# Kernel optimization log

Measured on AMD Instinct MI355X. Metric: run time of the kernel, lower is better.

## Reference

```python
import jax, jax.numpy as jnp
import numpy as np

N_HEAD = 16


def setup_inputs() -> dict:
    key = jax.random.key(0)
    k1, k2, k3 = jax.random.split(key, 3)
    B, T, C = 2, 2048, 1024
    x = jax.random.normal(k1, (B, T, C), dtype=jnp.float32)
    w_attn = jax.random.normal(k2, (C, 3 * C), dtype=jnp.float32) * 0.02
    w_proj = jax.random.normal(k3, (C, C), dtype=jnp.float32) * 0.02
    return {"x": x, "w_attn": w_attn, "w_proj": w_proj}


def reference(x, w_attn, w_proj):
    B, T, C = x.shape
    H = N_HEAD
    D = C // H
    qkv = x @ w_attn  # [B, T, 3C]
    q, k, v = jnp.split(qkv, 3, axis=2)
    q = q.reshape(B, T, H, D)
    k = k.reshape(B, T, H, D)
    v = v.reshape(B, T, H, D)
    scale = 1.0 / jnp.sqrt(jnp.asarray(D, dtype=x.dtype))
    # Full T x T score matrix, matching the 'standard_attention' path.
    att = jnp.einsum('bthd,bshd->bhts', q, k) * scale  # [B, H, T, T]
    causal = jnp.tril(jnp.ones((T, T), dtype=bool))
    att = jnp.where(causal[None, None, :, :], att, jnp.asarray(-jnp.inf, dtype=att.dtype))
    att = jax.nn.softmax(att, axis=-1)
    # dropout_p is False (== 0.0) in the original module, so no dropout applied.
    y = jnp.einsum('bhts,bshd->bthd', att, v)  # [B, T, H, D]
    y = y.reshape(B, T, C)
    return y @ w_proj
```

## Files before the change

kernel.cpp:

```cpp
#include <hip/hip_runtime.h>
#include <hip/hip_bf16.h>
#include <math.h>

#define BB 2
#define TT 2048
#define HH 16
#define DD 64
#define CC 1024
#define C3 3072

typedef __attribute__((ext_vector_type(8))) short bf16x8;
typedef __attribute__((ext_vector_type(4))) short bf16x4;
typedef __attribute__((ext_vector_type(4))) float f32x4;
typedef __attribute__((ext_vector_type(2))) unsigned int u32x2;

__device__ __forceinline__ unsigned short f2bf(float f) {
  union { float f; unsigned u; } v; v.f = f;
  unsigned r = v.u + 0x7fffu + ((v.u >> 16) & 1u);
  return (unsigned short)(r >> 16);
}
__device__ __forceinline__ unsigned pack2bf(float a, float b) {
  __hip_bfloat162 h = __float22bfloat162_rn(make_float2(a, b));
  union { __hip_bfloat162 h; unsigned u; } cv; cv.h = h;
  return cv.u;
}

__device__ __forceinline__ void async_cp16(const void* g, void* l) {
  __builtin_amdgcn_global_load_lds(
      (const __attribute__((address_space(1))) void*)g,
      (__attribute__((address_space(3))) void*)l, 16, 0, 0);
}

__global__ __launch_bounds__(256)
void prep(const float* __restrict__ x, const float* __restrict__ w_attn,
          const float* __restrict__ w_proj, unsigned short* __restrict__ xb,
          unsigned short* __restrict__ wat, unsigned short* __restrict__ wpt) {
  __shared__ __align__(16) float Ts[64][68];
  const int bx = blockIdx.x, tid = threadIdx.x;
  if (bx < 1024) {
    int i = bx * 256 + tid;
#pragma unroll
    for (int it = 0; it < 4; ++it, i += 262144) {
      const float4 v = ((const float4*)x)[i];
      bf16x4 o = {(short)f2bf(v.x), (short)f2bf(v.y),
                  (short)f2bf(v.z), (short)f2bf(v.w)};
      ((bf16x4*)xb)[i] = o;
    }
    return;
  }
  const float* W;
  unsigned short* WT;
  int Nd, bound, n0, k0;
  float s;
  if (bx < 1792) {
    const int bid = bx - 1024;
    W = w_attn; WT = wat; Nd = 3072; bound = 1024; s = 0.18033688f;
    n0 = (bid % 48) * 64; k0 = (bid / 48) * 64;
  } else {
    const int bid = bx - 1792;
    W = w_proj; WT = wpt; Nd = 1024; bound = 0; s = 1.0f;
    n0 = (bid % 16) * 64; k0 = (bid / 16) * 64;
  }
  const int rl = tid >> 4, c4 = tid & 15;
#pragma unroll
  for (int it = 0; it < 4; ++it) {
    const int r = it * 16 + rl;
    *(float4*)&Ts[r][c4 * 4] =
        *(const float4*)(W + (size_t)(k0 + r) * Nd + n0 + c4 * 4);
  }
  __syncthreads();
#pragma unroll
  for (int it = 0; it < 4; ++it) {
    const int n = it * 16 + rl;
    const float sc = (n0 + n < bound) ? s : 1.0f;
    bf16x4 o = {(short)f2bf(Ts[c4 * 4 + 0][n] * sc),
                (short)f2bf(Ts[c4 * 4 + 1][n] * sc),
                (short)f2bf(Ts[c4 * 4 + 2][n] * sc),
                (short)f2bf(Ts[c4 * 4 + 3][n] * sc)};
    *(bf16x4*)(WT + (size_t)(n0 + n) * CC + k0 + c4 * 4) = o;
  }
}

__global__ __launch_bounds__(256, 3)
void gemm_qkv(const unsigned short* __restrict__ A,
              const unsigned short* __restrict__ BT,
              unsigned short* __restrict__ Cb,
              unsigned short* __restrict__ Vout) {
  __shared__ __align__(16) unsigned short As[2 * 128 * 32];
  __shared__ __align__(16) unsigned short Bs[2 * 128 * 32];

  const int tid = threadIdx.x;
  const int w = tid >> 6, lane = tid & 63;
  const int l15 = lane & 15, quad = lane >> 4;
  const int wm = w >> 1, wn = w & 1;
  const int row0 = blockIdx.y * 128, col0 = blockIdx.x * 128;

  const int ca0 = tid, ca1 = tid + 256;
  const int ra0 = ca0 >> 2, ka0 = ((ca0 & 3) ^ ((ca0 >> 3) & 3)) * 8;
  const int ra1 = ca1 >> 2, ka1 = ((ca1 & 3) ^ ((ca1 >> 3) & 3)) * 8;
  const unsigned short* gA0 = A + (size_t)(row0 + ra0) * CC + ka0;
  const unsigned short* gA1 = A + (size_t)(row0 + ra1) * CC + ka1;
  const unsigned short* gB0 = BT + (size_t)(col0 + ra0) * CC + ka0;
  const unsigned short* gB1 = BT + (size_t)(col0 + ra1) * CC + ka1;
  const int la0 = tid * 16, la1 = tid * 16 + 4096;

  const int fro = l15 * 64 + 16 * (quad ^ ((l15 >> 1) & 3));

  f32x4 acc[4][4];
#pragma unroll
  for (int i = 0; i < 4; ++i)
#pragma unroll
    for (int j = 0; j < 4; ++j) acc[i][j] = (f32x4){0.f, 0.f, 0.f, 0.f};

  async_cp16(gA0, (char*)As + la0);
  async_cp16(gA1, (char*)As + la1);
  async_cp16(gB0, (char*)Bs + la0);
  async_cp16(gB1, (char*)Bs + la1);

  for (int i = 0; i < 32; ++i) {
    const int cur = i & 1;
    __syncthreads();

    if (i + 1 < 32) {
      const int k1 = (i + 1) * 32;
      const int ab = (cur ^ 1) * 8192;
      async_cp16(gA0 + k1, (char*)As + ab + la0);
      async_cp16(gA1 + k1, (char*)As + ab + la1);
      async_cp16(gB0 + k1, (char*)Bs + ab + la0);
      async_cp16(gB1 + k1, (char*)Bs + ab + la1);
    }

    const char* fA = (const char*)As + cur * 8192 + wm * 4096 + fro;
    const char* fB = (const char*)Bs + cur * 8192 + wn * 4096 + fro;

    bf16x8 af[4], bf[4];
#pragma unroll
    for (int mt = 0; mt < 4; ++mt) af[mt] = *(const bf16x8*)(fA + mt * 1024);
#pragma unroll
    for (int nt = 0; nt < 4; ++nt) bf[nt] = *(const bf16x8*)(fB + nt * 1024);
#pragma unroll
    for (int mt = 0; mt < 4; ++mt)
#pragma unroll
      for (int nt = 0; nt < 4; ++nt)
        acc[mt][nt] = __builtin_amdgcn_mfma_f32_16x16x32_bf16(
            af[mt], bf[nt], acc[mt][nt], 0, 0, 0);
  }

  if (col0 >= 2048) {
#pragma unroll
    for (int mt = 0; mt < 4; ++mt) {
      const int rbase = row0 + wm * 64 + mt * 16 + quad * 4;
      const int bq = rbase >> 11, t0 = rbase & 2047;
#pragma unroll
      for (int nt = 0; nt < 4; ++nt) {
        const int d = col0 + wn * 64 + nt * 16 + l15 - 2048;
        bf16x4 o = {(short)f2bf(acc[mt][nt][0]), (short)f2bf(acc[mt][nt][1]),
                    (short)f2bf(acc[mt][nt][2]), (short)f2bf(acc[mt][nt][3])};
        *(bf16x4*)(Vout + (((size_t)(bq << 10) + d) << 11) + t0) = o;
      }
    }
  } else {
#pragma unroll
    for (int mt = 0; mt < 4; ++mt) {
      const int rbase = row0 + wm * 64 + mt * 16 + quad * 4;
#pragma unroll
      for (int r = 0; r < 4; ++r) {
        unsigned short* cr =
            Cb + (size_t)(rbase + r) * C3 + col0 + wn * 64 + l15;
#pragma unroll
        for (int nt = 0; nt < 4; ++nt) cr[nt * 16] = f2bf(acc[mt][nt][r]);
      }
    }
  }
}

__global__ __launch_bounds__(256, 2)
void gemm_out(const unsigned short* __restrict__ A,
              const unsigned short* __restrict__ BT,
              float* __restrict__ Cf) {
  __shared__ __align__(16) unsigned short As[2 * 64 * 64];
  __shared__ __align__(16) unsigned short Bs[2 * 128 * 64];

  const int tid = threadIdx.x;
  const int w = tid >> 6, lane = tid & 63;
  const int l15 = lane & 15, quad = lane >> 4;
  const int wm = w >> 1, wn = w & 1;
  const int row0 = blockIdx.y * 64, col0 = blockIdx.x * 128;

  const int ca0 = tid, ca1 = tid + 256;
  const int ra0 = ca0 >> 3, ka0 = ((ca0 & 7) ^ ((ca0 >> 3) & 7)) * 8;
  const int ra1 = ca1 >> 3, ka1 = ((ca1 & 7) ^ ((ca1 >> 3) & 7)) * 8;
  const unsigned short* gA0 = A + (size_t)(row0 + ra0) * CC + ka0;
  const unsigned short* gA1 = A + (size_t)(row0 + ra1) * CC + ka1;
  const unsigned short* gB[4];
  int lb[4];
#pragma unroll
  for (int t = 0; t < 4; ++t) {
    const int c = tid + t * 256;
    const int rb = c >> 3, kb = ((c & 7) ^ ((c >> 3) & 7)) * 8;
    gB[t] = BT + (size_t)(col0 + rb) * CC + kb;
    lb[t] = c * 16;
  }
  const int la0 = tid * 16, la1 = tid * 16 + 4096;

  const int fro = l15 * 128 + ((quad ^ (l15 & 7)) << 4);

  f32x4 acc[2][4];
#pragma unroll
  for (int i = 0; i < 2; ++i)
#pragma unroll
    for (int j = 0; j < 4; ++j) acc[i][j] = (f32x4){0.f, 0.f, 0.f, 0.f};

  async_cp16(gA0, (char*)As + la0);
  async_cp16(gA1, (char*)As + la1);
#pragma unroll
  for (int t = 0; t < 4; ++t) async_cp16(gB[t], (char*)Bs + lb[t]);

  for (int i = 0; i < 16; ++i) {
    const int cur = i & 1;
    __syncthreads();

    if (i + 1 < 16) {
      const int k1 = (i + 1) * 64;
      const int ab = (cur ^ 1) * 8192, bb = (cur ^ 1) * 16384;
      async_cp16(gA0 + k1, (char*)As + ab + la0);
      async_cp16(gA1 + k1, (char*)As + ab + la1);
#pragma unroll
      for (int t = 0; t < 4; ++t) async_cp16(gB[t] + k1, (char*)Bs + bb + lb[t]);
    }

    const char* fA = (const char*)As + cur * 8192 + wm * 4096 + fro;
    const char* fB = (const char*)Bs + cur * 16384 + wn * 8192 + fro;

#pragma unroll
    for (int kh = 0; kh < 2; ++kh) {
      const int xo = kh * 64;
      bf16x8 af[2], bf[4];
#pragma unroll
      for (int mt = 0; mt < 2; ++mt)
        af[mt] = *(const bf16x8*)(fA + mt * 2048 + ((fro + xo) & 127) - (fro & 127));
#pragma unroll
      for (int nt = 0; nt < 4; ++nt)
        bf[nt] = *(const bf16x8*)(fB + nt * 2048 + ((fro + xo) & 127) - (fro & 127));
#pragma unroll
      for (int mt = 0; mt < 2; ++mt)
#pragma unroll
        for (int nt = 0; nt < 4; ++nt)
          acc[mt][nt] = __builtin_amdgcn_mfma_f32_16x16x32_bf16(
              af[mt], bf[nt], acc[mt][nt], 0, 0, 0);
    }
  }

#pragma unroll
  for (int mt = 0; mt < 2; ++mt) {
    const int rbase = row0 + wm * 32 + mt * 16 + quad * 4;
#pragma unroll
    for (int r = 0; r < 4; ++r) {
      float* cr = Cf + (size_t)(rbase + r) * CC + col0 + wn * 64 + l15;
#pragma unroll
      for (int nt = 0; nt < 4; ++nt) cr[nt * 16] = acc[mt][nt][r];
    }
  }
}

__global__ __launch_bounds__(256)
void attn_mfma(const unsigned short* __restrict__ qkvb,
               const unsigned short* __restrict__ vt,
               unsigned short* __restrict__ y) {
  const int n = blockIdx.x;
  const int bh = (n & 7) + 8 * ((n >> 3) & 3);
  const int qpair = n >> 5;
  const int b = bh >> 4, h = bh & 15;
  const int tid = threadIdx.x;
  const int w = tid >> 6;
  const int lane = tid & 63;
  const int l15 = lane & 15, quad = lane >> 4;

  __shared__ __align__(16) char Kb[2 * 8192];
  __shared__ __align__(16) char Vb[2 * 8192];
  __shared__ __align__(16) unsigned short Ps[4 * 16 * 72];
  char* psw = (char*)(Ps + w * 16 * 72);

  const int lr = lane >> 3;
  const int lc = lane & 7;
  const int srcoff = ((lc ^ lr) << 4);
  const char* ksrc = (const char*)qkvb + ((size_t)(b * TT) * C3 + 1024 + h * 64) * 2;
  const char* vsrc = (const char*)vt + ((size_t)(b * HH + h) * DD * TT) * 2;

  const int fro = l15 * 128 + ((quad ^ (l15 & 7)) << 4);

  const int psrow = l15 * 144;

  bf16x8 onesf;
#pragma unroll
  for (int jj = 0; jj < 8; ++jj) onesf[jj] = (short)0x3F80;

  for (int phase = 0; phase < 2; ++phase) {
    const int qt = phase == 0 ? 31 - qpair : qpair;

    if (phase) __syncthreads();

    const unsigned short* qrow =
        qkvb + (size_t)(b * TT + qt * 64 + w * 16 + l15) * C3 + h * DD;
    bf16x8 qf0 = *(const bf16x8*)(qrow + quad * 8);
    bf16x8 qf1 = *(const bf16x8*)(qrow + 32 + quad * 8);

    f32x4 O[4];
#pragma unroll
    for (int dt = 0; dt < 4; ++dt) O[dt] = (f32x4){0.f, 0.f, 0.f, 0.f};
    f32x4 lacc = (f32x4){0.f, 0.f, 0.f, 0.f};

#pragma unroll
    for (int i = 0; i < 2; ++i) {
      async_cp16(ksrc + (size_t)(w * 16 + i * 8 + lr) * (C3 * 2) + srcoff,
                 Kb + w * 2048 + i * 1024);
      async_cp16(vsrc + (size_t)(w * 16 + i * 8 + lr) * (TT * 2) + srcoff,
                 Vb + w * 2048 + i * 1024);
    }

    for (int j = 0; j <= qt; ++j) {
      const int cur = j & 1;
      __syncthreads();

      if (j < qt) {
        const int key1 = (j + 1) * 64;
        char* kd = Kb + (cur ^ 1) * 8192 + w * 2048;
        char* vd = Vb + (cur ^ 1) * 8192 + w * 2048;
#pragma unroll
        for (int i = 0; i < 2; ++i) {
          async_cp16(
              ksrc + (size_t)(key1 + w * 16 + i * 8 + lr) * (C3 * 2) + srcoff,
              kd + i * 1024);
          async_cp16(
              vsrc + (size_t)(w * 16 + i * 8 + lr) * (TT * 2) + key1 * 2 + srcoff,
              vd + i * 1024);
        }
      }

      const char* Kc = Kb + cur * 8192;
      const char* Vc = Vb + cur * 8192;

      f32x4 S[4];
#pragma unroll
      for (int ct = 0; ct < 4; ++ct) {
        bf16x8 k0 = *(const bf16x8*)(Kc + ct * 2048 + fro);
        bf16x8 k1 = *(const bf16x8*)(Kc + ct * 2048 + (fro ^ 64));
        f32x4 z = (f32x4){-12.f, -12.f, -12.f, -12.f};
        z = __builtin_amdgcn_mfma_f32_16x16x32_bf16(k0, qf0, z, 0, 0, 0);
        z = __builtin_amdgcn_mfma_f32_16x16x32_bf16(k1, qf1, z, 0, 0, 0);
        S[ct] = z;
      }

      if (j == qt) {
#pragma unroll
        for (int ct = 0; ct < 4; ++ct)
#pragma unroll
          for (int r = 0; r < 4; ++r)
            if (16 * ct + quad * 4 + r > w * 16 + l15) S[ct][r] = -INFINITY;
      }

#pragma unroll
      for (int ct = 0; ct < 4; ++ct) {
        u32x2 d;
        d[0] = pack2bf(__builtin_amdgcn_exp2f(S[ct][0]),
                       __builtin_amdgcn_exp2f(S[ct][1]));
        d[1] = pack2bf(__builtin_amdgcn_exp2f(S[ct][2]),
                       __builtin_amdgcn_exp2f(S[ct][3]));
        *(u32x2*)(psw + psrow + (((ct + l15) & 3) << 5) + quad * 8) = d;
      }

      bf16x8 pf0, pf1;
      {
        const int c0 = (quad >> 1), c1 = 2 + (quad >> 1);
        pf0 = *(const bf16x8*)(psw + psrow + (((c0 + l15) & 3) << 5) + ((quad & 1) << 4));
        pf1 = *(const bf16x8*)(psw + psrow + (((c1 + l15) & 3) << 5) + ((quad & 1) << 4));
      }

      lacc = __builtin_amdgcn_mfma_f32_16x16x32_bf16(onesf, pf0, lacc, 0, 0, 0);
      lacc = __builtin_amdgcn_mfma_f32_16x16x32_bf16(onesf, pf1, lacc, 0, 0, 0);
#pragma unroll
      for (int dt = 0; dt < 4; ++dt) {
        bf16x8 v0 = *(const bf16x8*)(Vc + dt * 2048 + fro);
        bf16x8 v1 = *(const bf16x8*)(Vc + dt * 2048 + (fro ^ 64));
        O[dt] = __builtin_amdgcn_mfma_f32_16x16x32_bf16(v0, pf0, O[dt], 0, 0, 0);
        O[dt] = __builtin_amdgcn_mfma_f32_16x16x32_bf16(v1, pf1, O[dt], 0, 0, 0);
      }
    }

    const float inv = 1.0f / lacc[0];
    unsigned short* yr =
        y + (size_t)(b * TT + qt * 64 + w * 16 + l15) * CC + h * DD + quad * 4;
#pragma unroll
    for (int dt = 0; dt < 4; ++dt) {
      bf16x4 o = {(short)f2bf(O[dt][0] * inv), (short)f2bf(O[dt][1] * inv),
                  (short)f2bf(O[dt][2] * inv), (short)f2bf(O[dt][3] * inv)};
      *(bf16x4*)(yr + dt * 16) = o;
    }
  }
}

extern "C" void kernel_launch(void* const* d_in, const int* in_sizes, int n_in,
                              void* d_out, int out_size, void* d_ws,
                              size_t ws_size, hipStream_t stream) {
  const float* x      = (const float*)d_in[0];
  const float* w_attn = (const float*)d_in[1];
  const float* w_proj = (const float*)d_in[2];
  float* out = (float*)d_out;

  unsigned short* xb   = (unsigned short*)d_ws;
  unsigned short* wat  = xb + (size_t)4096 * 1024;
  unsigned short* wpt  = wat + (size_t)3072 * 1024;
  unsigned short* qkvb = wpt + (size_t)1024 * 1024;
  unsigned short* vt   = qkvb + (size_t)4096 * 3072;
  unsigned short* yb   = vt + (size_t)BB * HH * DD * TT;

  dim3 blk(256);

  prep<<<2048, blk, 0, stream>>>(x, w_attn, w_proj, xb, wat, wpt);

  gemm_qkv<<<dim3(C3 / 128, (BB * TT) / 128), blk, 0, stream>>>(
      xb, wat, qkvb, vt);

  attn_mfma<<<dim3(512, 1, 1), blk, 0, stream>>>(qkvb, vt, yb);

  gemm_out<<<dim3(CC / 128, (BB * TT) / 64), blk, 0, stream>>>(yb, wpt, out);
}
```

Baseline: 170.2 us.

## Split attention keys across warps with register K/V loads and LDS reduction

Restructures the attention kernel so each warp handles all 64 query rows of the tile but only every fourth 32-key chunk. K and V fragments come straight from global memory into registers, with K double-buffered in registers, replacing the shared-memory async copy pipeline and its per-iteration block barriers. The four warps' partial O and row sums are then combined through a two-level shared-memory reduction before warp 0 normalises and writes the output. This removes a __syncthreads per key tile but raises register pressure (O is now 4x4 accumulators per warp), adds an end-of-phase reduction, and makes every warp read K/V from global memory rather than sharing a single staged copy.

```diff
diff --git a/kernel.cpp b/kernel.cpp
--- a/kernel.cpp
+++ b/kernel.cpp
@@ -263,7 +263,72 @@
   }
 }
 
-__global__ __launch_bounds__(256)
+__device__ __forceinline__ void attn_chunk(
+    const int c, const int qt, const int l15, const int quad,
+    const bf16x8 (&kf)[2][2], const bf16x8 (&qf)[4][2], const bf16x8 onesf,
+    const unsigned short* __restrict__ vbase, char* psw, const int psrow,
+    f32x4 (&O)[4][4], f32x4 (&lacc)[4]) {
+  bf16x8 vf[4];
+#pragma unroll
+  for (int dt = 0; dt < 4; ++dt)
+    vf[dt] = *(const bf16x8*)(vbase + (size_t)dt * 16 * TT + 32 * c);
+
+  f32x4 S[2][4];
+#pragma unroll
+  for (int ks = 0; ks < 2; ++ks)
+#pragma unroll
+    for (int qs = 0; qs < 4; ++qs) {
+      f32x4 z = (f32x4){-12.f, -12.f, -12.f, -12.f};
+      z = __builtin_amdgcn_mfma_f32_16x16x32_bf16(kf[ks][0], qf[qs][0], z, 0, 0, 0);
+      z = __builtin_amdgcn_mfma_f32_16x16x32_bf16(kf[ks][1], qf[qs][1], z, 0, 0, 0);
+      S[ks][qs] = z;
+    }
+
+  if (c >= 2 * qt) {
+#pragma unroll
+    for (int ks = 0; ks < 2; ++ks)
+#pragma unroll
+      for (int qs = 0; qs < 4; ++qs)
+#pragma unroll
+        for (int r = 0; r < 4; ++r)
+          if (32 * c + ks * 16 + quad * 4 + r > qt * 64 + qs * 16 + l15)
+            S[ks][qs][r] = -INFINITY;
+  }
+
+#pragma unroll
+  for (int ks = 0; ks < 2; ++ks)
+#pragma unroll
+    for (int qs = 0; qs < 4; ++qs) {
+      u32x2 d;
+      d[0] = pack2bf(__builtin_amdgcn_exp2f(S[ks][qs][0]),
+                     __builtin_amdgcn_exp2f(S[ks][qs][1]));
+      d[1] = pack2bf(__builtin_amdgcn_exp2f(S[ks][qs][2]),
+                     __builtin_amdgcn_exp2f(S[ks][qs][3]));
+      *(u32x2*)(psw + qs * 2304 + psrow + (((ks + l15) & 3) << 5) + quad * 8) = d;
+    }
+
+#pragma unroll
+  for (int qs = 0; qs < 4; ++qs) {
+    const bf16x8 pf = *(const bf16x8*)(psw + qs * 2304 + psrow +
+                                       ((((quad >> 1) + l15) & 3) << 5) +
+                                       ((quad & 1) << 4));
+    lacc[qs] = __builtin_amdgcn_mfma_f32_16x16x32_bf16(onesf, pf, lacc[qs], 0, 0, 0);
+#pragma unroll
+    for (int dt = 0; dt < 4; ++dt)
+      O[dt][qs] = __builtin_amdgcn_mfma_f32_16x16x32_bf16(vf[dt], pf, O[dt][qs], 0, 0, 0);
+  }
+}
+
+#define LOADK(dst, cc)                                                   \
+  do {                                                                   \
+    const unsigned short* kp = kbase + (size_t)(32 * (cc)) * C3;         \
+    dst[0][0] = *(const bf16x8*)(kp);                                    \
+    dst[0][1] = *(const bf16x8*)(kp + 32);                               \
+    dst[1][0] = *(const bf16x8*)(kp + 16 * C3);                          \
+    dst[1][1] = *(const bf16x8*)(kp + 16 * C3 + 32);                     \
+  } while (0)
+
+__global__ __launch_bounds__(256, 2)
 void attn_mfma(const unsigned short* __restrict__ qkvb,
                const unsigned short* __restrict__ vt,
                unsigned short* __restrict__ y) {
@@ -276,125 +341,125 @@
   const int lane = tid & 63;
   const int l15 = lane & 15, quad = lane >> 4;
 
-  __shared__ __align__(16) char Kb[2 * 8192];
-  __shared__ __align__(16) char Vb[2 * 8192];
-  __shared__ __align__(16) unsigned short Ps[4 * 16 * 72];
-  char* psw = (char*)(Ps + w * 16 * 72);
-
-  const int lr = lane >> 3;
-  const int lc = lane & 7;
-  const int srcoff = ((lc ^ lr) << 4);
-  const char* ksrc = (const char*)qkvb + ((size_t)(b * TT) * C3 + 1024 + h * 64) * 2;
-  const char* vsrc = (const char*)vt + ((size_t)(b * HH + h) * DD * TT) * 2;
-
-  const int fro = l15 * 128 + ((quad ^ (l15 & 7)) << 4);
-
+  __shared__ __align__(16) unsigned short Ps[4 * 4 * 16 * 72];
+  __shared__ __align__(16) float Red[2][16][256];
+  __shared__ float Red2[2][4][16];
+
+  char* psw = (char*)Ps + w * (4 * 2304);
   const int psrow = l15 * 144;
+  const int epoff = l15 * 64 + ((quad ^ (l15 & 3)) << 4);
+
+  const unsigned short* kbase =
+      qkvb + (size_t)(b * TT + l15) * C3 + 1024 + h * DD + quad * 8;
+  const unsigned short* vbase =
+      vt + (size_t)(bh * DD + l15) * TT + quad * 8;
 
   bf16x8 onesf;
 #pragma unroll
   for (int jj = 0; jj < 8; ++jj) onesf[jj] = (short)0x3F80;
 
   for (int phase = 0; phase < 2; ++phase) {
-    const int qt = phase == 0 ? 31 - qpair : qpair;
-
-    if (phase) __syncthreads();
-
-    const unsigned short* qrow =
-        qkvb + (size_t)(b * TT + qt * 64 + w * 16 + l15) * C3 + h * DD;
-    bf16x8 qf0 = *(const bf16x8*)(qrow + quad * 8);
-    bf16x8 qf1 = *(const bf16x8*)(qrow + 32 + quad * 8);
-
-    f32x4 O[4];
-#pragma unroll
-    for (int dt = 0; dt < 4; ++dt) O[dt] = (f32x4){0.f, 0.f, 0.f, 0.f};
-    f32x4 lacc = (f32x4){0.f, 0.f, 0.f, 0.f};
-
-#pragma unroll
-    for (int i = 0; i < 2; ++i) {
-      async_cp16(ksrc + (size_t)(w * 16 + i * 8 + lr) * (C3 * 2) + srcoff,
-                 Kb + w * 2048 + i * 1024);
-      async_cp16(vsrc + (size_t)(w * 16 + i * 8 + lr) * (TT * 2) + srcoff,
-                 Vb + w * 2048 + i * 1024);
-    }
-
-    for (int j = 0; j <= qt; ++j) {
-      const int cur = j & 1;
-      __syncthreads();
-
-      if (j < qt) {
-        const int key1 = (j + 1) * 64;
-        char* kd = Kb + (cur ^ 1) * 8192 + w * 2048;
-        char* vd = Vb + (cur ^ 1) * 8192 + w * 2048;
-#pragma unroll
-        for (int i = 0; i < 2; ++i) {
-          async_cp16(
-              ksrc + (size_t)(key1 + w * 16 + i * 8 + lr) * (C3 * 2) + srcoff,
-              kd + i * 1024);
-          async_cp16(
-              vsrc + (size_t)(w * 16 + i * 8 + lr) * (TT * 2) + key1 * 2 + srcoff,
-              vd + i * 1024);
+    const int qt = phase ? qpair : 31 - qpair;
+    const int nc = 2 * (qt + 1);
+
+    const unsigned short* qbase =
+        qkvb + (size_t)(b * TT + qt * 64 + l15) * C3 + h * DD + quad * 8;
+    bf16x8 qf[4][2];
+#pragma unroll
+    for (int qs = 0; qs < 4; ++qs)
+#pragma unroll
+      for (int kh = 0; kh < 2; ++kh)
+        qf[qs][kh] = *(const bf16x8*)(qbase + qs * 16 * C3 + kh * 32);
+
+    f32x4 O[4][4];
+    f32x4 lacc[4];
+#pragma unroll
+    for (int dt = 0; dt < 4; ++dt)
+#pragma unroll
+      for (int qs = 0; qs < 4; ++qs) O[dt][qs] = (f32x4){0.f, 0.f, 0.f, 0.f};
+#pragma unroll
+    for (int qs = 0; qs < 4; ++qs) lacc[qs] = (f32x4){0.f, 0.f, 0.f, 0.f};
+
+    bf16x8 kfA[2][2], kfB[2][2];
+    int c = w;
+    if (c < nc) {
+      LOADK(kfA, c);
+      while (true) {
+        int cn = c + 4;
+        if (cn < nc) LOADK(kfB, cn);
+        attn_chunk(c, qt, l15, quad, kfA, qf, onesf, vbase, psw, psrow, O, lacc);
+        c = cn;
+        if (c >= nc) break;
+        cn = c + 4;
+        if (cn < nc) LOADK(kfA, cn);
+        attn_chunk(c, qt, l15, quad, kfB, qf, onesf, vbase, psw, psrow, O, lacc);
+        c = cn;
+        if (c >= nc) break;
+      }
+    }
+
+    __syncthreads();
+    if (w & 1) {
+      char* rs = (char*)Red + (w >> 1) * 16384;
+#pragma unroll
+      for (int dt = 0; dt < 4; ++dt)
+#pragma unroll
+        for (int qs = 0; qs < 4; ++qs)
+          *(f32x4*)(rs + (dt * 4 + qs) * 1024 + epoff) = O[dt][qs];
+      if (quad == 0) {
+#pragma unroll
+        for (int qs = 0; qs < 4; ++qs) Red2[w >> 1][qs][l15] = lacc[qs][0];
+      }
+    }
+    __syncthreads();
+    float lsum[4];
+#pragma unroll
+    for (int qs = 0; qs < 4; ++qs) lsum[qs] = lacc[qs][0];
+    if (!(w & 1)) {
+      char* rs = (char*)Red + (w >> 1) * 16384;
+#pragma unroll
+      for (int dt = 0; dt < 4; ++dt)
+#pragma unroll
+        for (int qs = 0; qs < 4; ++qs)
+          O[dt][qs] += *(const f32x4*)(rs + (dt * 4 + qs) * 1024 + epoff);
+#pragma unroll
+      for (int qs = 0; qs < 4; ++qs) lsum[qs] += Red2[w >> 1][qs][l15];
+    }
+    __syncthreads();
+    if (w == 2) {
+      char* rs = (char*)Red;
+#pragma unroll
+      for (int dt = 0; dt < 4; ++dt)
+#pragma unroll
+        for (int qs = 0; qs < 4; ++qs)
+          *(f32x4*)(rs + (dt * 4 + qs) * 1024 + epoff) = O[dt][qs];
+      if (quad == 0) {
+#pragma unroll
+        for (int qs = 0; qs < 4; ++qs) Red2[0][qs][l15] = lsum[qs];
+      }
+    }
+    __syncthreads();
+    if (w == 0) {
+      char* rs = (char*)Red;
+#pragma unroll
+      for (int dt = 0; dt < 4; ++dt)
+#pragma unroll
+        for (int qs = 0; qs < 4; ++qs)
+          O[dt][qs] += *(const f32x4*)(rs + (dt * 4 + qs) * 1024 + epoff);
+      unsigned short* yr =
+          y + (size_t)(b * TT + qt * 64 + l15) * CC + h * DD + quad * 4;
+#pragma unroll
+      for (int qs = 0; qs < 4; ++qs) {
+        const float inv = 1.0f / (lsum[qs] + Red2[0][qs][l15]);
+#pragma unroll
+        for (int dt = 0; dt < 4; ++dt) {
+          bf16x4 o = {(short)f2bf(O[dt][qs][0] * inv),
+                      (short)f2bf(O[dt][qs][1] * inv),
+                      (short)f2bf(O[dt][qs][2] * inv),
+                      (short)f2bf(O[dt][qs][3] * inv)};
+          *(bf16x4*)(yr + (size_t)qs * 16 * CC + dt * 16) = o;
         }
       }
-
-      const char* Kc = Kb + cur * 8192;
-      const char* Vc = Vb + cur * 8192;
-
-      f32x4 S[4];
-#pragma unroll
-      for (int ct = 0; ct < 4; ++ct) {
-        bf16x8 k0 = *(const bf16x8*)(Kc + ct * 2048 + fro);
-        bf16x8 k1 = *(const bf16x8*)(Kc + ct * 2048 + (fro ^ 64));
-        f32x4 z = (f32x4){-12.f, -12.f, -12.f, -12.f};
-        z = __builtin_amdgcn_mfma_f32_16x16x32_bf16(k0, qf0, z, 0, 0, 0);
-        z = __builtin_amdgcn_mfma_f32_16x16x32_bf16(k1, qf1, z, 0, 0, 0);
-        S[ct] = z;
-      }
-
-      if (j == qt) {
-#pragma unroll
-        for (int ct = 0; ct < 4; ++ct)
-#pragma unroll
-          for (int r = 0; r < 4; ++r)
-            if (16 * ct + quad * 4 + r > w * 16 + l15) S[ct][r] = -INFINITY;
-      }
-
-#pragma unroll
-      for (int ct = 0; ct < 4; ++ct) {
-        u32x2 d;
-        d[0] = pack2bf(__builtin_amdgcn_exp2f(S[ct][0]),
-                       __builtin_amdgcn_exp2f(S[ct][1]));
-        d[1] = pack2bf(__builtin_amdgcn_exp2f(S[ct][2]),
-                       __builtin_amdgcn_exp2f(S[ct][3]));
-        *(u32x2*)(psw + psrow + (((ct + l15) & 3) << 5) + quad * 8) = d;
-      }
-
-      bf16x8 pf0, pf1;
-      {
-        const int c0 = (quad >> 1), c1 = 2 + (quad >> 1);
-        pf0 = *(const bf16x8*)(psw + psrow + (((c0 + l15) & 3) << 5) + ((quad & 1) << 4));
-        pf1 = *(const bf16x8*)(psw + psrow + (((c1 + l15) & 3) << 5) + ((quad & 1) << 4));
-      }
-
-      lacc = __builtin_amdgcn_mfma_f32_16x16x32_bf16(onesf, pf0, lacc, 0, 0, 0);
-      lacc = __builtin_amdgcn_mfma_f32_16x16x32_bf16(onesf, pf1, lacc, 0, 0, 0);
-#pragma unroll
-      for (int dt = 0; dt < 4; ++dt) {
-        bf16x8 v0 = *(const bf16x8*)(Vc + dt * 2048 + fro);
-        bf16x8 v1 = *(const bf16x8*)(Vc + dt * 2048 + (fro ^ 64));
-        O[dt] = __builtin_amdgcn_mfma_f32_16x16x32_bf16(v0, pf0, O[dt], 0, 0, 0);
-        O[dt] = __builtin_amdgcn_mfma_f32_16x16x32_bf16(v1, pf1, O[dt], 0, 0, 0);
-      }
-    }
-
-    const float inv = 1.0f / lacc[0];
-    unsigned short* yr =
-        y + (size_t)(b * TT + qt * 64 + w * 16 + l15) * CC + h * DD + quad * 4;
-#pragma unroll
-    for (int dt = 0; dt < 4; ++dt) {
-      bf16x4 o = {(short)f2bf(O[dt][0] * inv), (short)f2bf(O[dt][1] * inv),
-                  (short)f2bf(O[dt][2] * inv), (short)f2bf(O[dt][3] * inv)};
-      *(bf16x4*)(yr + dt * 16) = o;
     }
   }
 }
```

After: 173.8 us. +2.2%, slower.

## Use 128-query attention blocks with 8 waves instead of paired 64-query phases

Applied to the files above, without the earlier changes.

The attention kernel now launches 512-thread blocks where 8 waves each own 16 query rows, covering a 128-row query tile that shares one K/V stream. This replaces the two-phase pairing of a long and a short 64-row tile per block. Each wave loads only one 8-row slice of K/V per stage, and waves past their causal limit skip compute. Blocks are ordered so that heavy and light query tiles are interleaved. The aim is to halve K/V traffic per query and raise occupancy, at the cost of idle waves on the diagonal tiles and coarser per-block load balance.

```diff
diff --git a/kernel.cpp b/kernel.cpp
--- a/kernel.cpp
+++ b/kernel.cpp
@@ -263,13 +263,14 @@
   }
 }
 
-__global__ __launch_bounds__(256)
+__global__ __launch_bounds__(512, 4)
 void attn_mfma(const unsigned short* __restrict__ qkvb,
                const unsigned short* __restrict__ vt,
                unsigned short* __restrict__ y) {
   const int n = blockIdx.x;
   const int bh = (n & 7) + 8 * ((n >> 3) & 3);
-  const int qpair = n >> 5;
+  const int m = n >> 5;
+  const int qb = (m < 8) ? m : 23 - m;
   const int b = bh >> 4, h = bh & 15;
   const int tid = threadIdx.x;
   const int w = tid >> 6;
@@ -278,8 +279,10 @@
 
   __shared__ __align__(16) char Kb[2 * 8192];
   __shared__ __align__(16) char Vb[2 * 8192];
-  __shared__ __align__(16) unsigned short Ps[4 * 16 * 72];
-  char* psw = (char*)(Ps + w * 16 * 72);
+  __shared__ __align__(16) unsigned short Ps[8 * 16 * 72];
+
+  char* psw = (char*)Ps + w * 2304;
+  const int psrow = l15 * 144;
 
   const int lr = lane >> 3;
   const int lc = lane & 7;
@@ -289,113 +292,99 @@
 
   const int fro = l15 * 128 + ((quad ^ (l15 & 7)) << 4);
 
-  const int psrow = l15 * 144;
-
   bf16x8 onesf;
 #pragma unroll
   for (int jj = 0; jj < 8; ++jj) onesf[jj] = (short)0x3F80;
 
-  for (int phase = 0; phase < 2; ++phase) {
-    const int qt = phase == 0 ? 31 - qpair : qpair;
-
-    if (phase) __syncthreads();
-
-    const unsigned short* qrow =
-        qkvb + (size_t)(b * TT + qt * 64 + w * 16 + l15) * C3 + h * DD;
-    bf16x8 qf0 = *(const bf16x8*)(qrow + quad * 8);
-    bf16x8 qf1 = *(const bf16x8*)(qrow + 32 + quad * 8);
-
-    f32x4 O[4];
-#pragma unroll
-    for (int dt = 0; dt < 4; ++dt) O[dt] = (f32x4){0.f, 0.f, 0.f, 0.f};
-    f32x4 lacc = (f32x4){0.f, 0.f, 0.f, 0.f};
-
-#pragma unroll
-    for (int i = 0; i < 2; ++i) {
-      async_cp16(ksrc + (size_t)(w * 16 + i * 8 + lr) * (C3 * 2) + srcoff,
-                 Kb + w * 2048 + i * 1024);
-      async_cp16(vsrc + (size_t)(w * 16 + i * 8 + lr) * (TT * 2) + srcoff,
-                 Vb + w * 2048 + i * 1024);
-    }
-
-    for (int j = 0; j <= qt; ++j) {
-      const int cur = j & 1;
-      __syncthreads();
-
-      if (j < qt) {
-        const int key1 = (j + 1) * 64;
-        char* kd = Kb + (cur ^ 1) * 8192 + w * 2048;
-        char* vd = Vb + (cur ^ 1) * 8192 + w * 2048;
-#pragma unroll
-        for (int i = 0; i < 2; ++i) {
-          async_cp16(
-              ksrc + (size_t)(key1 + w * 16 + i * 8 + lr) * (C3 * 2) + srcoff,
-              kd + i * 1024);
-          async_cp16(
-              vsrc + (size_t)(w * 16 + i * 8 + lr) * (TT * 2) + key1 * 2 + srcoff,
-              vd + i * 1024);
-        }
-      }
-
-      const char* Kc = Kb + cur * 8192;
-      const char* Vc = Vb + cur * 8192;
-
-      f32x4 S[4];
-#pragma unroll
-      for (int ct = 0; ct < 4; ++ct) {
-        bf16x8 k0 = *(const bf16x8*)(Kc + ct * 2048 + fro);
-        bf16x8 k1 = *(const bf16x8*)(Kc + ct * 2048 + (fro ^ 64));
-        f32x4 z = (f32x4){-12.f, -12.f, -12.f, -12.f};
-        z = __builtin_amdgcn_mfma_f32_16x16x32_bf16(k0, qf0, z, 0, 0, 0);
-        z = __builtin_amdgcn_mfma_f32_16x16x32_bf16(k1, qf1, z, 0, 0, 0);
-        S[ct] = z;
-      }
-
-      if (j == qt) {
-#pragma unroll
-        for (int ct = 0; ct < 4; ++ct)
-#pragma unroll
-          for (int r = 0; r < 4; ++r)
-            if (16 * ct + quad * 4 + r > w * 16 + l15) S[ct][r] = -INFINITY;
-      }
-
-#pragma unroll
-      for (int ct = 0; ct < 4; ++ct) {
-        u32x2 d;
-        d[0] = pack2bf(__builtin_amdgcn_exp2f(S[ct][0]),
-                       __builtin_amdgcn_exp2f(S[ct][1]));
-        d[1] = pack2bf(__builtin_amdgcn_exp2f(S[ct][2]),
-                       __builtin_amdgcn_exp2f(S[ct][3]));
-        *(u32x2*)(psw + psrow + (((ct + l15) & 3) << 5) + quad * 8) = d;
-      }
-
-      bf16x8 pf0, pf1;
-      {
-        const int c0 = (quad >> 1), c1 = 2 + (quad >> 1);
-        pf0 = *(const bf16x8*)(psw + psrow + (((c0 + l15) & 3) << 5) + ((quad & 1) << 4));
-        pf1 = *(const bf16x8*)(psw + psrow + (((c1 + l15) & 3) << 5) + ((quad & 1) << 4));
-      }
-
-      lacc = __builtin_amdgcn_mfma_f32_16x16x32_bf16(onesf, pf0, lacc, 0, 0, 0);
-      lacc = __builtin_amdgcn_mfma_f32_16x16x32_bf16(onesf, pf1, lacc, 0, 0, 0);
-#pragma unroll
-      for (int dt = 0; dt < 4; ++dt) {
-        bf16x8 v0 = *(const bf16x8*)(Vc + dt * 2048 + fro);
-        bf16x8 v1 = *(const bf16x8*)(Vc + dt * 2048 + (fro ^ 64));
-        O[dt] = __builtin_amdgcn_mfma_f32_16x16x32_bf16(v0, pf0, O[dt], 0, 0, 0);
-        O[dt] = __builtin_amdgcn_mfma_f32_16x16x32_bf16(v1, pf1, O[dt], 0, 0, 0);
-      }
-    }
-
-    const float inv = 1.0f / lacc[0];
-    unsigned short* yr =
-        y + (size_t)(b * TT + qt * 64 + w * 16 + l15) * CC + h * DD + quad * 4;
+  const int nt = 2 * qb + 2;
+  const int qrow_my = qb * 128 + w * 16 + l15;
+  const int jlast = (qb * 128 + w * 16 + 15) >> 6;
+
+  const unsigned short* qrow =
+      qkvb + (size_t)(b * TT + qb * 128 + w * 16 + l15) * C3 + h * DD;
+  bf16x8 qf0 = *(const bf16x8*)(qrow + quad * 8);
+  bf16x8 qf1 = *(const bf16x8*)(qrow + 32 + quad * 8);
+
+  f32x4 O[4];
+#pragma unroll
+  for (int dt = 0; dt < 4; ++dt) O[dt] = (f32x4){0.f, 0.f, 0.f, 0.f};
+  f32x4 lacc = (f32x4){0.f, 0.f, 0.f, 0.f};
+
+  async_cp16(ksrc + (size_t)(w * 8 + lr) * (C3 * 2) + srcoff, Kb + w * 1024);
+  async_cp16(vsrc + (size_t)(w * 8 + lr) * (TT * 2) + srcoff, Vb + w * 1024);
+
+  for (int j = 0; j < nt; ++j) {
+    const int cur = j & 1;
+    __syncthreads();
+
+    if (j + 1 < nt) {
+      const int key1 = (j + 1) * 64;
+      async_cp16(ksrc + (size_t)(key1 + w * 8 + lr) * (C3 * 2) + srcoff,
+                 Kb + (cur ^ 1) * 8192 + w * 1024);
+      async_cp16(vsrc + (size_t)(w * 8 + lr) * (TT * 2) + key1 * 2 + srcoff,
+                 Vb + (cur ^ 1) * 8192 + w * 1024);
+    }
+
+    if (j > jlast) continue;
+
+    const char* Kc = Kb + cur * 8192;
+    const char* Vc = Vb + cur * 8192;
+
+    f32x4 S[4];
+#pragma unroll
+    for (int ct = 0; ct < 4; ++ct) {
+      bf16x8 k0 = *(const bf16x8*)(Kc + ct * 2048 + fro);
+      bf16x8 k1 = *(const bf16x8*)(Kc + ct * 2048 + (fro ^ 64));
+      f32x4 z = (f32x4){-12.f, -12.f, -12.f, -12.f};
+      z = __builtin_amdgcn_mfma_f32_16x16x32_bf16(k0, qf0, z, 0, 0, 0);
+      z = __builtin_amdgcn_mfma_f32_16x16x32_bf16(k1, qf1, z, 0, 0, 0);
+      S[ct] = z;
+    }
+
+    if (j == jlast) {
+#pragma unroll
+      for (int ct = 0; ct < 4; ++ct)
+#pragma unroll
+        for (int r = 0; r < 4; ++r)
+          if (64 * j + 16 * ct + quad * 4 + r > qrow_my) S[ct][r] = -INFINITY;
+    }
+
+#pragma unroll
+    for (int ct = 0; ct < 4; ++ct) {
+      u32x2 d;
+      d[0] = pack2bf(__builtin_amdgcn_exp2f(S[ct][0]),
+                     __builtin_amdgcn_exp2f(S[ct][1]));
+      d[1] = pack2bf(__builtin_amdgcn_exp2f(S[ct][2]),
+                     __builtin_amdgcn_exp2f(S[ct][3]));
+      *(u32x2*)(psw + psrow + (((ct + l15) & 3) << 5) + quad * 8) = d;
+    }
+
+    bf16x8 pf0, pf1;
+    {
+      const int c0 = (quad >> 1), c1 = 2 + (quad >> 1);
+      pf0 = *(const bf16x8*)(psw + psrow + (((c0 + l15) & 3) << 5) + ((quad & 1) << 4));
+      pf1 = *(const bf16x8*)(psw + psrow + (((c1 + l15) & 3) << 5) + ((quad & 1) << 4));
+    }
+
+    lacc = __builtin_amdgcn_mfma_f32_16x16x32_bf16(onesf, pf0, lacc, 0, 0, 0);
+    lacc = __builtin_amdgcn_mfma_f32_16x16x32_bf16(onesf, pf1, lacc, 0, 0, 0);
 #pragma unroll
     for (int dt = 0; dt < 4; ++dt) {
-      bf16x4 o = {(short)f2bf(O[dt][0] * inv), (short)f2bf(O[dt][1] * inv),
-                  (short)f2bf(O[dt][2] * inv), (short)f2bf(O[dt][3] * inv)};
-      *(bf16x4*)(yr + dt * 16) = o;
-    }
+      bf16x8 v0 = *(const bf16x8*)(Vc + dt * 2048 + fro);
+      bf16x8 v1 = *(const bf16x8*)(Vc + dt * 2048 + (fro ^ 64));
+      O[dt] = __builtin_amdgcn_mfma_f32_16x16x32_bf16(v0, pf0, O[dt], 0, 0, 0);
+      O[dt] = __builtin_amdgcn_mfma_f32_16x16x32_bf16(v1, pf1, O[dt], 0, 0, 0);
+    }
+  }
+
+  const float inv = 1.0f / lacc[0];
+  unsigned short* yr =
+      y + (size_t)(b * TT + qb * 128 + w * 16 + l15) * CC + h * DD + quad * 4;
+#pragma unroll
+  for (int dt = 0; dt < 4; ++dt) {
+    bf16x4 o = {(short)f2bf(O[dt][0] * inv), (short)f2bf(O[dt][1] * inv),
+                (short)f2bf(O[dt][2] * inv), (short)f2bf(O[dt][3] * inv)};
+    *(bf16x4*)(yr + dt * 16) = o;
   }
 }
 
@@ -421,7 +410,7 @@
   gemm_qkv<<<dim3(C3 / 128, (BB * TT) / 128), blk, 0, stream>>>(
       xb, wat, qkvb, vt);
 
-  attn_mfma<<<dim3(512, 1, 1), blk, 0, stream>>>(qkvb, vt, yb);
+  attn_mfma<<<dim3(512, 1, 1), dim3(512), 0, stream>>>(qkvb, vt, yb);
 
   gemm_out<<<dim3(CC / 128, (BB * TT) / 64), blk, 0, stream>>>(yb, wpt, out);
 }
```

Measured after the change: 170.8 us. Within noise of the previous version (+0.4%).
